# Optimization experiments

Measured on AMD Instinct MI355X. Metric: run time of the kernel, lower is better.

## Reference

```python
import jax, jax.numpy as jnp
import numpy as np

N = 50000          # nodes
E = 800000         # edges (avg degree 16)
FEAT = 128         # self.feat_dim
MAX_SPK = 3
SPK_DIM = 16
SPA_DIM = 16
OUT = 64


def _lin(key, din, dout):
    kw, kb = jax.random.split(key)
    w = jax.random.normal(kw, (din, dout), dtype=jnp.float32) * (1.0 / np.sqrt(din))
    b = jax.random.normal(kb, (dout,), dtype=jnp.float32) * 0.01
    return w, b


def setup_inputs() -> dict:
    key = jax.random.key(0)
    ks = jax.random.split(key, 16)
    D = 7 * FEAT + 5  # 901
    x = jax.random.normal(ks[0], (N, D), dtype=jnp.float32)
    # last column is a speaker count in {1..4} (clamped to max 3 in forward)
    num_spk = jax.random.randint(ks[1], (N,), 1, 5).astype(jnp.float32)
    x = x.at[:, -1].set(num_spk)
    edge_index = jax.random.randint(ks[2], (2, E), 0, N, dtype=jnp.int32)
    edge_attr = jnp.zeros((E,), dtype=jnp.int32)  # all pass the (==111)|(==0) filter

    speaker_w, speaker_b = _lin(ks[3], MAX_SPK, SPK_DIM)
    spatial_w, spatial_b = _lin(ks[4], 4, SPA_DIM)
    # face_trans params
    f1_w, f1_b = _lin(ks[5], FEAT, OUT)
    f2_w, f2_b = _lin(ks[6], FEAT + SPK_DIM + SPA_DIM, OUT)
    fe_w, fe_b = _lin(ks[7], 2 * OUT, 2)
    # face_body_trans params
    g1_w, g1_b = _lin(ks[8], FEAT, OUT)
    g2_w, g2_b = _lin(ks[9], FEAT + SPK_DIM + SPA_DIM, OUT)
    ge_w, ge_b = _lin(ks[10], 2 * OUT, 2)
    return dict(x=x, edge_index=edge_index, edge_attr=edge_attr,
                speaker_w=speaker_w, speaker_b=speaker_b,
                spatial_w=spatial_w, spatial_b=spatial_b,
                f1_w=f1_w, f1_b=f1_b, f2_w=f2_w, f2_b=f2_b, fe_w=fe_w, fe_b=fe_b,
                g1_w=g1_w, g1_b=g1_b, g2_w=g2_w, g2_b=g2_b, ge_w=ge_w, ge_b=ge_b)


def _edge_conv(h, src, dst, valid, ew, eb):
    # PyG EdgeConv (aggr='max'): out_i = max_j MLP([x_i, x_j - x_i])
    hi = h[dst]                                   # [E, 64]
    hj = h[src]                                   # [E, 64]
    msg = jnp.concatenate([hi, hj - hi], axis=1) @ ew + eb  # [E, 2]
    msg = jnp.where(valid[:, None], msg, -jnp.inf)
    out = jax.ops.segment_max(msg, dst, num_segments=h.shape[0])
    return jnp.where(jnp.isfinite(out), out, 0.0)  # empty segments -> 0 (PyG fill)


def reference(x, edge_index, edge_attr,
              speaker_w, speaker_b, spatial_w, spatial_b,
              f1_w, f1_b, f2_w, f2_b, fe_w, fe_b,
              g1_w, g1_b, g2_w, g2_b, ge_w, ge_b):
    valid = (edge_attr == 111) | (edge_attr == 0)
    src, dst = edge_index[0], edge_index[1]

    # speaker-count embedding: one_hot(clamp(x[:,-1]-1, max=2)) -> Linear(3,16)
    spk_idx = jnp.minimum(x[:, -1] - 1.0, MAX_SPK - 1).astype(jnp.int32)
    spk = jax.nn.one_hot(spk_idx, MAX_SPK, dtype=x.dtype) @ speaker_w + speaker_b
    spa = x[:, -5:-1] @ spatial_w + spatial_b

    def block(feat, fc1_w, fc1_b, fc2_w, fc2_b, ew, eb):
        # dropout p=0.9 is identity in eval mode
        h = (feat @ fc1_w + fc1_b) + (jnp.concatenate([feat, spk, spa], axis=1) @ fc2_w + fc2_b)
        return _edge_conv(h, src, dst, valid, ew, eb)

    o_face = block(x[:, :FEAT], f1_w, f1_b, f2_w, f2_b, fe_w, fe_b)
    o_body = block(x[:, FEAT:2 * FEAT], g1_w, g1_b, g2_w, g2_b, ge_w, ge_b)
    return o_face + o_body
```

## Files before the change

### kernel.cpp

```cpp
#include <hip/hip_runtime.h>
#include <hip/hip_bf16.h>
#include <math.h>

#define ROWLEN 901
#define CNTSTRIDE 8
#define NB_SC 512
#define ZB 96

__global__ __launch_bounds__(256) void k_compose(
    const float* __restrict__ spkw, const float* __restrict__ spkb,
    const float* __restrict__ spaw, const float* __restrict__ spab,
    const float* __restrict__ f1w, const float* __restrict__ f1b,
    const float* __restrict__ f2w, const float* __restrict__ f2b,
    const float* __restrict__ few, const float* __restrict__ feb,
    const float* __restrict__ g1w, const float* __restrict__ g1b,
    const float* __restrict__ g2w, const float* __restrict__ g2b,
    const float* __restrict__ gew, const float* __restrict__ geb,
    float* __restrict__ C, float* __restrict__ Sp,
    float* __restrict__ Tab, float* __restrict__ Cst,
    uint4* __restrict__ cntz, int nCntQuads, int* __restrict__ spillcnt)
{
    const int t = threadIdx.x;

    if (blockIdx.x >= 17) {
        const int zid = blockIdx.x - 17;
        if (zid == 0 && t == 0) *spillcnt = 0;
        const uint4 z = make_uint4(0u, 0u, 0u, 0u);
        for (int i = zid * 256 + t; i < nCntQuads; i += ZB * 256)
            cntz[i] = z;
        return;
    }

    if (blockIdx.x < 16) {
        const int row = blockIdx.x * 16 + (t >> 4);
        const int kk  = t & 15;
        const int blk = row >> 7;
        const int fr  = row & 127;
        const float* w1 = blk ? g1w : f1w;
        const float* w2 = blk ? g2w : f2w;
        const float* e  = blk ? gew : few;

        const float4 wa = *(const float4*)(w1 + fr * 64 + kk * 4);
        const float4 wb = *(const float4*)(w2 + fr * 64 + kk * 4);
        const float wv[4] = {wa.x + wb.x, wa.y + wb.y, wa.z + wb.z, wa.w + wb.w};

        float a0 = 0.f, a1 = 0.f, a2 = 0.f, a3 = 0.f;
        #pragma unroll
        for (int j = 0; j < 4; ++j) {
            const int k = kk * 4 + j;
            const float eb0 = e[(64 + k) * 2 + 0];
            const float eb1 = e[(64 + k) * 2 + 1];
            const float ea0 = e[k * 2 + 0] - eb0;
            const float ea1 = e[k * 2 + 1] - eb1;
            a0 += wv[j] * ea0; a1 += wv[j] * ea1;
            a2 += wv[j] * eb0; a3 += wv[j] * eb1;
        }
        #pragma unroll
        for (int m = 1; m <= 8; m <<= 1) {
            a0 += __shfl_xor(a0, m, 64);
            a1 += __shfl_xor(a1, m, 64);
            a2 += __shfl_xor(a2, m, 64);
            a3 += __shfl_xor(a3, m, 64);
        }
        if (kk == 0) {
            C[row * 4 + 0] = a0; C[row * 4 + 1] = a1;
            C[row * 4 + 2] = a2; C[row * 4 + 3] = a3;
        }
        return;
    }

    __shared__ float sEW[2][256];
    __shared__ float sUV[2][2][2][16][2];
    __shared__ float sBE[8][8];

    sEW[0][t] = few[t];
    sEW[1][t] = gew[t];
    __syncthreads();

    {
        const int c    = t & 1;
        const int k16  = (t >> 1) & 15;
        const int role = (t >> 5) & 1;
        const int blk  = (t >> 6) & 1;
        const int isV  = (t >> 7) & 1;
        const float* w2 = blk ? g2w : f2w;
        const float* e  = sEW[blk];
        const int row = (isV ? 144 : 128) + k16;
        float acc = 0.f;
        #pragma unroll
        for (int k4 = 0; k4 < 16; ++k4) {
            const float4 w = *(const float4*)(w2 + row * 64 + k4 * 4);
            const float wv[4] = {w.x, w.y, w.z, w.w};
            #pragma unroll
            for (int j = 0; j < 4; ++j) {
                const int k = k4 * 4 + j;
                const float ev = role ? e[(64 + k) * 2 + c]
                                      : (e[k * 2 + c] - e[(64 + k) * 2 + c]);
                acc += wv[j] * ev;
            }
        }
        sUV[isV][blk][role][k16][c] = acc;
    }

    if (t < 64) {
        const int combo = t >> 3;
        const int part  = t & 7;
        const int c = combo & 1, role = (combo >> 1) & 1, blk = combo >> 2;
        const float* b1 = blk ? g1b : f1b;
        const float* b2 = blk ? g2b : f2b;
        const float* e  = sEW[blk];
        float acc = 0.f;
        #pragma unroll
        for (int j = 0; j < 8; ++j) {
            const int k = part * 8 + j;
            const float ev = role ? e[(64 + k) * 2 + c]
                                  : (e[k * 2 + c] - e[(64 + k) * 2 + c]);
            acc += (b1[k] + b2[k]) * ev;
        }
        sBE[combo][part] = acc;
    }
    __syncthreads();

    if (t < 24) {
        const int blk = t / 12, rem = t % 12;
        const int idx = rem >> 2, q = rem & 3;
        const int role = q >> 1, c = q & 1;
        float acc = 0.f;
        #pragma unroll
        for (int k = 0; k < 16; ++k)
            acc += spkw[idx * 16 + k] * sUV[0][blk][role][k][c];
        Tab[blk * 12 + idx * 4 + q] = acc;
    } else if (t >= 32 && t < 64) {
        const int u = t - 32;
        const int blk = u >> 4, rem = u & 15;
        const int r = rem >> 2, q = rem & 3;
        const int role = q >> 1, c = q & 1;
        float acc = 0.f;
        #pragma unroll
        for (int k = 0; k < 16; ++k)
            acc += spaw[r * 16 + k] * sUV[1][blk][role][k][c];
        Sp[blk * 16 + r * 4 + q] = acc;
    } else if (t >= 64 && t < 72) {
        const int u = t - 64;
        const int blk = u >> 2, q = u & 3;
        const int role = q >> 1, c = q & 1;
        const float* ebv = blk ? geb : feb;
        float acc = (role == 0) ? ebv[c] : 0.f;
        #pragma unroll
        for (int k = 0; k < 16; ++k) {
            acc += spkb[k] * sUV[0][blk][role][k][c];
            acc += spab[k] * sUV[1][blk][role][k][c];
        }
        #pragma unroll
        for (int p = 0; p < 8; ++p) acc += sBE[u][p];
        Cst[blk * 4 + q] = acc;
    }
}

__global__ __launch_bounds__(256) void k_fused(
    const float* __restrict__ x,
    const float* __restrict__ C, const float* __restrict__ Sp,
    const float* __restrict__ Tab, const float* __restrict__ Cst,
    float4* __restrict__ Adat, float4* __restrict__ Bdat, int nnodes,
    const int* __restrict__ ei, const int* __restrict__ ea,
    int* __restrict__ cnt, int* __restrict__ bucket,
    int* __restrict__ spillcnt, int* __restrict__ spill,
    int nedges, int cap)
{
    if (blockIdx.x < NB_SC) {
        for (int e = blockIdx.x * 256 + threadIdx.x; e < nedges; e += NB_SC * 256) {
            const int attr = ea[e];
            if (!(attr == 0 || attr == 111)) continue;
            const int s = ei[e];
            const int d = ei[nedges + e];
            const int pos = atomicAdd(cnt + (size_t)d * CNTSTRIDE, 1);
            if (pos < cap) {
                bucket[(size_t)d * cap + pos] = s;
            } else {
                const int sp = atomicAdd(spillcnt, 1);
                spill[2 * sp + 0] = d;
                spill[2 * sp + 1] = s;
            }
        }
        return;
    }

    const int wave = threadIdx.x >> 6;
    const int lane = threadIdx.x & 63;
    const int node = (blockIdx.x - NB_SC) * 4 + wave;
    if (node >= nnodes) return;

    const float* xr = x + (size_t)node * ROWLEN;
    const int half = lane >> 5;
    const int l32  = lane & 31;
    const float* xh = xr + half * 128;
    const float4* C4 = (const float4*)C;

    float xs0 = 0.f, xs1 = 0.f, xs2 = 0.f, xs3 = 0.f, xspk = 0.f;
    if (lane == 0) {
        xs0 = xr[896]; xs1 = xr[897]; xs2 = xr[898]; xs3 = xr[899];
        xspk = xr[900];
    }

    float a0 = 0.f, a1 = 0.f, a2 = 0.f, a3 = 0.f;
    #pragma unroll
    for (int k = 0; k < 4; ++k) {
        const int el = l32 + 32 * k;
        const float v = xh[el];
        const float4 cr = C4[half * 128 + el];
        a0 += v * cr.x; a1 += v * cr.y; a2 += v * cr.z; a3 += v * cr.w;
    }

    #pragma unroll
    for (int m = 16; m >= 1; m >>= 1) {
        a0 += __shfl_xor(a0, m, 64);
        a1 += __shfl_xor(a1, m, 64);
        a2 += __shfl_xor(a2, m, 64);
        a3 += __shfl_xor(a3, m, 64);
    }
    const float b0 = __shfl(a0, 32, 64);
    const float b1 = __shfl(a1, 32, 64);
    const float b2 = __shfl(a2, 32, 64);
    const float b3 = __shfl(a3, 32, 64);

    if (lane == 0) {
        const float xs[4] = {xs0, xs1, xs2, xs3};
        int idx = (int)fminf(xspk - 1.0f, 2.0f);
        idx = idx < 0 ? 0 : (idx > 2 ? 2 : idx);

        const float pq[2][4] = {{a0, a1, a2, a3}, {b0, b1, b2, b3}};
        float av[4], bv[4];
        #pragma unroll
        for (int blk = 0; blk < 2; ++blk) {
            #pragma unroll
            for (int c = 0; c < 2; ++c) {
                float ea_ = Tab[blk * 12 + idx * 4 + c] + Cst[blk * 4 + c];
                float eb_ = Tab[blk * 12 + idx * 4 + 2 + c] + Cst[blk * 4 + 2 + c];
                #pragma unroll
                for (int r = 0; r < 4; ++r) {
                    ea_ += xs[r] * Sp[blk * 16 + r * 4 + c];
                    eb_ += xs[r] * Sp[blk * 16 + r * 4 + 2 + c];
                }
                av[blk * 2 + c] = pq[blk][c] + ea_;
                bv[blk * 2 + c] = pq[blk][2 + c] + eb_;
            }
        }
        Adat[node] = make_float4(av[0], av[1], av[2], av[3]);
        Bdat[node] = make_float4(bv[0], bv[1], bv[2], bv[3]);
    }
}

__global__ __launch_bounds__(256) void k_gather(
    const float4* __restrict__ Adat, const float4* __restrict__ Bdat,
    const int* __restrict__ cnt, const int* __restrict__ bucket,
    const int* __restrict__ spillcnt, const int* __restrict__ spill,
    float* __restrict__ out, int nnodes, int cap)
{
    const int t = blockIdx.x * blockDim.x + threadIdx.x;
    const int n = t >> 2, sub = t & 3;
    if (n >= nnodes) return;
    int c = cnt[(size_t)n * CNTSTRIDE]; if (c > cap) c = cap;

    float m0 = -INFINITY, m1 = -INFINITY, m2 = -INFINITY, m3 = -INFINITY;
    const int* row = bucket + (size_t)n * cap;
    int i = sub;
    int s_next = (i < c) ? row[i] : 0;
    while (i < c) {
        const int s = s_next;
        i += 4;
        if (i < c) s_next = row[i];
        const float4 b = Bdat[s];
        m0 = fmaxf(m0, b.x); m1 = fmaxf(m1, b.y);
        m2 = fmaxf(m2, b.z); m3 = fmaxf(m3, b.w);
    }

    const int ns = *spillcnt;
    if (ns > 0) {
        for (int j = sub; j < ns; j += 4) {
            if (spill[2 * j] == n) {
                const float4 b = Bdat[spill[2 * j + 1]];
                m0 = fmaxf(m0, b.x); m1 = fmaxf(m1, b.y);
                m2 = fmaxf(m2, b.z); m3 = fmaxf(m3, b.w);
            }
        }
    }

    #pragma unroll
    for (int msk = 1; msk <= 2; msk <<= 1) {
        m0 = fmaxf(m0, __shfl_xor(m0, msk, 64));
        m1 = fmaxf(m1, __shfl_xor(m1, msk, 64));
        m2 = fmaxf(m2, __shfl_xor(m2, msk, 64));
        m3 = fmaxf(m3, __shfl_xor(m3, msk, 64));
    }
    if (sub == 0) {
        const float4 a = Adat[n];
        const float f0 = isfinite(m0) ? a.x + m0 : 0.f;
        const float f1 = isfinite(m1) ? a.y + m1 : 0.f;
        const float f2 = isfinite(m2) ? a.z + m2 : 0.f;
        const float f3 = isfinite(m3) ? a.w + m3 : 0.f;
        out[(size_t)n * 2 + 0] = f0 + f2;
        out[(size_t)n * 2 + 1] = f1 + f3;
    }
}

extern "C" void kernel_launch(void* const* d_in, const int* in_sizes, int n_in,
                              void* d_out, int out_size, void* d_ws, size_t ws_size,
                              hipStream_t stream) {
    const float* x    = (const float*)d_in[0];
    const int*   ei   = (const int*)d_in[1];
    const int*   ea   = (const int*)d_in[2];
    const float* spkw = (const float*)d_in[3];
    const float* spkb = (const float*)d_in[4];
    const float* spaw = (const float*)d_in[5];
    const float* spab = (const float*)d_in[6];
    const float* f1w  = (const float*)d_in[7];
    const float* f1b  = (const float*)d_in[8];
    const float* f2w  = (const float*)d_in[9];
    const float* f2b  = (const float*)d_in[10];
    const float* few  = (const float*)d_in[11];
    const float* feb  = (const float*)d_in[12];
    const float* g1w  = (const float*)d_in[13];
    const float* g1b  = (const float*)d_in[14];
    const float* g2w  = (const float*)d_in[15];
    const float* g2b  = (const float*)d_in[16];
    const float* gew  = (const float*)d_in[17];
    const float* geb  = (const float*)d_in[18];

    const int N = in_sizes[0] / ROWLEN;
    const int E = in_sizes[2];

    char* ws = (char*)d_ws;
    float*    C      = (float*)(ws + 0);
    float*    Sp     = (float*)(ws + 4096);
    float*    Tab    = (float*)(ws + 4096 + 128);
    float*    Cst    = (float*)(ws + 4096 + 256);
    size_t off = 16384;
    float4*   Adat   = (float4*)(ws + off);   off += (size_t)N * 16;
    float4*   Bdat   = (float4*)(ws + off);   off += (size_t)N * 16;
    size_t cntBytes  = (((size_t)N * CNTSTRIDE * 4 + 255) / 256) * 256;
    int*      cnt    = (int*)(ws + off);      off += cntBytes;
    int*      spillcnt = (int*)(ws + off);    off += 256;
    int*      spill  = (int*)(ws + off);      off += (((size_t)E * 8 + 255) / 256) * 256;
    int*      bucket = (int*)(ws + off);
    const size_t remain = ws_size > off ? ws_size - off : 0;
    size_t cap_sz = remain / ((size_t)N * 4);
    int CAP = cap_sz > 64 ? 64 : (int)cap_sz;

    const int nCntQuads = (int)(cntBytes / 16);

    k_compose<<<17 + ZB, 256, 0, stream>>>(spkw, spkb, spaw, spab,
                                           f1w, f1b, f2w, f2b, few, feb,
                                           g1w, g1b, g2w, g2b, gew, geb,
                                           C, Sp, Tab, Cst,
                                           (uint4*)cnt, nCntQuads, spillcnt);

    const int NB_ND = (N + 3) / 4;
    k_fused<<<NB_SC + NB_ND, 256, 0, stream>>>(x, C, Sp, Tab, Cst,
                                               Adat, Bdat, N,
                                               ei, ea, cnt, bucket,
                                               spillcnt, spill, E, CAP);

    k_gather<<<((size_t)N * 4 + 255) / 256, 256, 0, stream>>>(Adat, Bdat, cnt, bucket,
                                                              spillcnt, spill,
                                                              (float*)d_out, N, CAP);
}
```

Before: 314.8 us.

## Replace per-node global atomic bucketing with block-local binned edge partitioning

Edge scattering now groups edges into bins of 64 destination nodes. Each of 128 blocks counts per bin with shared-memory atomics and writes packed (src, local dst) entries into its own fixed sub-slot, instead of doing global atomics on per-node counters. The final kernel processes one bin per block, reducing maxima through shared-memory atomicMax on order-preserving encoded floats. This removes contended global atomics and the large per-node count zeroing. In exchange, overflow beyond 32 entries per block-bin goes to a spill list that every bin block scans linearly, and the bin data layout is sparse and can be large.

Measured after the change: 307.0 us. -2.5%, faster.

```diff
diff --git a/kernel.cpp b/kernel.cpp
--- a/kernel.cpp
+++ b/kernel.cpp
@@ -3,9 +3,23 @@
 #include <math.h>
 
 #define ROWLEN 901
-#define CNTSTRIDE 8
-#define NB_SC 512
+#define NEGENC 0x007FFFFFu
+#define GSH 6
+#define G (1 << GSH)
+#define MAXBINS 1024
+#define NB_A 128
+#define SUB 32
+#define BINCAP (NB_A * SUB)
 #define ZB 96
+
+__device__ __forceinline__ unsigned encf(float f) {
+    unsigned u = __float_as_uint(f);
+    return (u & 0x80000000u) ? ~u : (u | 0x80000000u);
+}
+__device__ __forceinline__ float decf(unsigned u) {
+    return (u & 0x80000000u) ? __uint_as_float(u ^ 0x80000000u)
+                             : __uint_as_float(~u);
+}
 
 __global__ __launch_bounds__(256) void k_compose(
     const float* __restrict__ spkw, const float* __restrict__ spkb,
@@ -18,7 +32,7 @@
     const float* __restrict__ gew, const float* __restrict__ geb,
     float* __restrict__ C, float* __restrict__ Sp,
     float* __restrict__ Tab, float* __restrict__ Cst,
-    uint4* __restrict__ cntz, int nCntQuads, int* __restrict__ spillcnt)
+    uint4* __restrict__ zq, int nZeroQuads, int* __restrict__ spillcnt)
 {
     const int t = threadIdx.x;
 
@@ -26,8 +40,8 @@
         const int zid = blockIdx.x - 17;
         if (zid == 0 && t == 0) *spillcnt = 0;
         const uint4 z = make_uint4(0u, 0u, 0u, 0u);
-        for (int i = zid * 256 + t; i < nCntQuads; i += ZB * 256)
-            cntz[i] = z;
+        for (int i = zid * 256 + t; i < nZeroQuads; i += ZB * 256)
+            zq[i] = z;
         return;
     }
 
@@ -163,31 +177,43 @@
     const float* __restrict__ Tab, const float* __restrict__ Cst,
     float4* __restrict__ Adat, float4* __restrict__ Bdat, int nnodes,
     const int* __restrict__ ei, const int* __restrict__ ea,
-    int* __restrict__ cnt, int* __restrict__ bucket,
+    int* __restrict__ binData, int* __restrict__ counts,
     int* __restrict__ spillcnt, int* __restrict__ spill,
-    int nedges, int cap)
+    int nedges, int nbins)
 {
-    if (blockIdx.x < NB_SC) {
-        for (int e = blockIdx.x * 256 + threadIdx.x; e < nedges; e += NB_SC * 256) {
+    __shared__ int sCnt[MAXBINS];
+
+    if (blockIdx.x < NB_A) {
+        for (int i = threadIdx.x; i < nbins; i += 256) sCnt[i] = 0;
+        __syncthreads();
+        const int chunk = (nedges + NB_A - 1) / NB_A;
+        const int e0 = blockIdx.x * chunk;
+        const int e1 = min(e0 + chunk, nedges);
+        for (int e = e0 + threadIdx.x; e < e1; e += 256) {
             const int attr = ea[e];
             if (!(attr == 0 || attr == 111)) continue;
             const int s = ei[e];
             const int d = ei[nedges + e];
-            const int pos = atomicAdd(cnt + (size_t)d * CNTSTRIDE, 1);
-            if (pos < cap) {
-                bucket[(size_t)d * cap + pos] = s;
+            const int bin = d >> GSH;
+            const int slot = atomicAdd(&sCnt[bin], 1);
+            if (slot < SUB) {
+                binData[(size_t)bin * BINCAP + blockIdx.x * SUB + slot] =
+                    s | ((d & (G - 1)) << 20);
             } else {
                 const int sp = atomicAdd(spillcnt, 1);
                 spill[2 * sp + 0] = d;
                 spill[2 * sp + 1] = s;
             }
         }
+        __syncthreads();
+        for (int i = threadIdx.x; i < nbins; i += 256)
+            counts[blockIdx.x * nbins + i] = sCnt[i];
         return;
     }
 
     const int wave = threadIdx.x >> 6;
     const int lane = threadIdx.x & 63;
-    const int node = (blockIdx.x - NB_SC) * 4 + wave;
+    const int node = (blockIdx.x - NB_A) * 4 + wave;
     if (node >= nnodes) return;
 
     const float* xr = x + (size_t)node * ROWLEN;
@@ -250,56 +276,71 @@
     }
 }
 
-__global__ __launch_bounds__(256) void k_gather(
+__global__ __launch_bounds__(256) void k_final(
     const float4* __restrict__ Adat, const float4* __restrict__ Bdat,
-    const int* __restrict__ cnt, const int* __restrict__ bucket,
+    const int* __restrict__ binData, const int* __restrict__ counts,
     const int* __restrict__ spillcnt, const int* __restrict__ spill,
-    float* __restrict__ out, int nnodes, int cap)
+    float* __restrict__ out, int nnodes, int nbins)
 {
-    const int t = blockIdx.x * blockDim.x + threadIdx.x;
-    const int n = t >> 2, sub = t & 3;
-    if (n >= nnodes) return;
-    int c = cnt[(size_t)n * CNTSTRIDE]; if (c > cap) c = cap;
-
-    float m0 = -INFINITY, m1 = -INFINITY, m2 = -INFINITY, m3 = -INFINITY;
-    const int* row = bucket + (size_t)n * cap;
-    int i = sub;
-    int s_next = (i < c) ? row[i] : 0;
-    while (i < c) {
-        const int s = s_next;
-        i += 4;
-        if (i < c) s_next = row[i];
-        const float4 b = Bdat[s];
-        m0 = fmaxf(m0, b.x); m1 = fmaxf(m1, b.y);
-        m2 = fmaxf(m2, b.z); m3 = fmaxf(m3, b.w);
-    }
-
-    const int ns = *spillcnt;
-    if (ns > 0) {
-        for (int j = sub; j < ns; j += 4) {
-            if (spill[2 * j] == n) {
+    const int bin = blockIdx.x;
+    const int t = threadIdx.x;
+    __shared__ unsigned sMax[G * 4];
+    __shared__ int sC[NB_A];
+    __shared__ int sNs;
+
+    if (t < G * 4) sMax[t] = NEGENC;
+    if (t < NB_A) sC[t] = counts[t * nbins + bin];
+    if (t == 0) sNs = *spillcnt;
+    __syncthreads();
+
+    #pragma unroll
+    for (int r = 0; r < NB_A / 32; ++r) {
+        const int slice = r * 32 + (t >> 3);
+        int c = sC[slice]; if (c > SUB) c = SUB;
+        const int* base = binData + (size_t)bin * BINCAP + slice * SUB;
+        for (int j = (t & 7); j < c; j += 8) {
+            const int entry = base[j];
+            const int s  = entry & 0xFFFFF;
+            const int dl = (entry >> 20) & (G - 1);
+            const float4 b = Bdat[s];
+            atomicMax(&sMax[dl * 4 + 0], encf(b.x));
+            atomicMax(&sMax[dl * 4 + 1], encf(b.y));
+            atomicMax(&sMax[dl * 4 + 2], encf(b.z));
+            atomicMax(&sMax[dl * 4 + 3], encf(b.w));
+        }
+    }
+
+    if (sNs > 0) {
+        const int lo = bin << GSH, hi = lo + G;
+        for (int j = t; j < sNs; j += 256) {
+            const int d = spill[2 * j];
+            if (d >= lo && d < hi) {
                 const float4 b = Bdat[spill[2 * j + 1]];
-                m0 = fmaxf(m0, b.x); m1 = fmaxf(m1, b.y);
-                m2 = fmaxf(m2, b.z); m3 = fmaxf(m3, b.w);
+                const int dl = d - lo;
+                atomicMax(&sMax[dl * 4 + 0], encf(b.x));
+                atomicMax(&sMax[dl * 4 + 1], encf(b.y));
+                atomicMax(&sMax[dl * 4 + 2], encf(b.z));
+                atomicMax(&sMax[dl * 4 + 3], encf(b.w));
             }
         }
     }
-
-    #pragma unroll
-    for (int msk = 1; msk <= 2; msk <<= 1) {
-        m0 = fmaxf(m0, __shfl_xor(m0, msk, 64));
-        m1 = fmaxf(m1, __shfl_xor(m1, msk, 64));
-        m2 = fmaxf(m2, __shfl_xor(m2, msk, 64));
-        m3 = fmaxf(m3, __shfl_xor(m3, msk, 64));
-    }
-    if (sub == 0) {
-        const float4 a = Adat[n];
-        const float f0 = isfinite(m0) ? a.x + m0 : 0.f;
-        const float f1 = isfinite(m1) ? a.y + m1 : 0.f;
-        const float f2 = isfinite(m2) ? a.z + m2 : 0.f;
-        const float f3 = isfinite(m3) ? a.w + m3 : 0.f;
-        out[(size_t)n * 2 + 0] = f0 + f2;
-        out[(size_t)n * 2 + 1] = f1 + f3;
+    __syncthreads();
+
+    if (t < G) {
+        const int n = (bin << GSH) + t;
+        if (n < nnodes) {
+            const float m0 = decf(sMax[t * 4 + 0]);
+            const float m1 = decf(sMax[t * 4 + 1]);
+            const float m2 = decf(sMax[t * 4 + 2]);
+            const float m3 = decf(sMax[t * 4 + 3]);
+            const float4 a = Adat[n];
+            const float f0 = isfinite(m0) ? a.x + m0 : 0.f;
+            const float f1 = isfinite(m1) ? a.y + m1 : 0.f;
+            const float f2 = isfinite(m2) ? a.z + m2 : 0.f;
+            const float f3 = isfinite(m3) ? a.w + m3 : 0.f;
+            out[(size_t)n * 2 + 0] = f0 + f2;
+            out[(size_t)n * 2 + 1] = f1 + f3;
+        }
     }
 }
 
@@ -328,6 +369,7 @@
 
     const int N = in_sizes[0] / ROWLEN;
     const int E = in_sizes[2];
+    const int nbins = (N + G - 1) >> GSH;
 
     char* ws = (char*)d_ws;
     float*    C      = (float*)(ws + 0);
@@ -337,30 +379,27 @@
     size_t off = 16384;
     float4*   Adat   = (float4*)(ws + off);   off += (size_t)N * 16;
     float4*   Bdat   = (float4*)(ws + off);   off += (size_t)N * 16;
-    size_t cntBytes  = (((size_t)N * CNTSTRIDE * 4 + 255) / 256) * 256;
-    int*      cnt    = (int*)(ws + off);      off += cntBytes;
+    size_t countsBytes = (((size_t)NB_A * nbins * 4 + 255) / 256) * 256;
+    int*      counts = (int*)(ws + off);      off += countsBytes;
     int*      spillcnt = (int*)(ws + off);    off += 256;
     int*      spill  = (int*)(ws + off);      off += (((size_t)E * 8 + 255) / 256) * 256;
-    int*      bucket = (int*)(ws + off);
-    const size_t remain = ws_size > off ? ws_size - off : 0;
-    size_t cap_sz = remain / ((size_t)N * 4);
-    int CAP = cap_sz > 64 ? 64 : (int)cap_sz;
-
-    const int nCntQuads = (int)(cntBytes / 16);
+    int*      binData = (int*)(ws + off);
+
+    const int nZeroQuads = (int)(countsBytes / 16);
 
     k_compose<<<17 + ZB, 256, 0, stream>>>(spkw, spkb, spaw, spab,
                                            f1w, f1b, f2w, f2b, few, feb,
                                            g1w, g1b, g2w, g2b, gew, geb,
                                            C, Sp, Tab, Cst,
-                                           (uint4*)cnt, nCntQuads, spillcnt);
+                                           (uint4*)counts, nZeroQuads, spillcnt);
 
     const int NB_ND = (N + 3) / 4;
-    k_fused<<<NB_SC + NB_ND, 256, 0, stream>>>(x, C, Sp, Tab, Cst,
-                                               Adat, Bdat, N,
-                                               ei, ea, cnt, bucket,
-                                               spillcnt, spill, E, CAP);
-
-    k_gather<<<((size_t)N * 4 + 255) / 256, 256, 0, stream>>>(Adat, Bdat, cnt, bucket,
-                                                              spillcnt, spill,
-                                                              (float*)d_out, N, CAP);
-}
+    k_fused<<<NB_A + NB_ND, 256, 0, stream>>>(x, C, Sp, Tab, Cst,
+                                              Adat, Bdat, N,
+                                              ei, ea, binData, counts,
+                                              spillcnt, spill, E, nbins);
+
+    k_final<<<nbins, 256, 0, stream>>>(Adat, Bdat, binData, counts,
+                                       spillcnt, spill,
+                                       (float*)d_out, N, nbins);
+}
```
